# Performance work log

Measured on AMD Instinct MI355X. Metric: run time of the kernel, lower is better.

The kernel has to match this reference:

```python
import jax, jax.numpy as jnp
import numpy as np

V, N, D, R, L, KS = 32000, 2048, 1024, 16, 4, 7
B, H = 2, 4 * 1024
GMIN, GMAX, ACAP = 0.85, 1.0, 1.0


def rmsnorm(x, w, eps=1e-6):
    return x * jax.lax.rsqrt(jnp.mean(x * x, axis=-1, keepdims=True) + eps) * w


def l2norm(x, eps=1e-8):
    return x / jnp.maximum(jnp.linalg.norm(x, axis=-1, keepdims=True), eps)


def mlp(x, w1, b1, w2, b2):
    return jax.nn.gelu(x @ w1 + b1) @ w2 + b2


def k1_block(h, nw, w1, b1, w2, b2):
    return h + mlp(rmsnorm(h, nw), w1, b1, w2, b2)


def causal_conv(h, kernel):
    # depthwise causal conv with shared 1D kernel; kernel[0] = current step
    n = h.shape[1]
    hp = jnp.pad(h, ((0, 0), (KS - 1, 0), (0, 0)))
    out = jnp.zeros_like(h)
    for k in range(KS):  # KS is small & static
        out = out + kernel[k] * hp[:, KS - 1 - k: KS - 1 - k + n, :]
    return out


def k2_layer(h, p):
    (u, v, dlog, alog, glog, kern, pw, pb, n1w, n2w, w1, b1, w2, b2) = p
    residual = h
    hn = rmsnorm(h, n1w)
    gate = jax.nn.sigmoid(glog)
    out = gate * causal_conv(hn, kern)
    # low-rank q/k
    q = l2norm(hn @ u)          # (B,N,R)
    k = l2norm(hn @ v)          # (B,N,R)
    gamma = GMIN + (GMAX - GMIN) * jax.nn.sigmoid(dlog)   # (R,)
    alpha = ACAP * jax.nn.sigmoid(alog)                   # (R,)
    qa = q * alpha
    pos = jnp.arange(h.shape[1])
    diff = jnp.maximum(pos[:, None] - pos[None, :], 0).astype(h.dtype)
    mask = (pos[:, None] >= pos[None, :]).astype(h.dtype)
    # per-rank causal decay matrix gamma_r^(i-j): (R,N,N)
    decay = jnp.exp(diff[None] * jnp.log(gamma)[:, None, None]) * mask[None]
    scores = jnp.einsum('bir,rij,bjr->bij', qa, decay, k)  # (B,N,N)
    out = out + jnp.einsum('bij,bjd->bid', scores, hn)
    out = out @ pw + pb
    h = residual + out
    h = h + mlp(rmsnorm(h, n2w), w1, b1, w2, b2)
    return h


def setup_inputs() -> dict:
    key = jax.random.key(0)
    ks = jax.random.split(key, 32)
    f32 = jnp.float32
    inp = {
        'tokens': jax.random.randint(ks[0], (B, N), 0, V),
        'emb_table': jax.random.normal(ks[1], (V, D), f32) * 0.02,
        'k1a_nw': jnp.ones((D,), f32),
        'k1a_w1': jax.random.normal(ks[2], (D, H), f32) * 0.02,
        'k1a_b1': jnp.zeros((H,), f32),
        'k1a_w2': jax.random.normal(ks[3], (H, D), f32) * 0.02,
        'k1a_b2': jnp.zeros((D,), f32),
        'k2_u': jax.random.normal(ks[4], (L, D, R), f32) * 0.05,
        'k2_v': jax.random.normal(ks[5], (L, D, R), f32) * 0.05,
        'k2_dlog': jax.random.normal(ks[6], (L, R), f32) * 0.5,
        'k2_alog': jnp.zeros((L, R), f32),
        'k2_glog': jnp.zeros((L,), f32),
        'k2_kern': jax.random.normal(ks[7], (L, KS), f32) * 0.1,
        'k2_pw': jax.random.normal(ks[8], (L, D, D), f32) * 0.02,
        'k2_pb': jnp.zeros((L, D), f32),
        'k2_n1w': jnp.ones((L, D), f32),
        'k2_n2w': jnp.ones((L, D), f32),
        'k2_w1': jax.random.normal(ks[9], (L, D, H), f32) * 0.02,
        'k2_b1': jnp.zeros((L, H), f32),
        'k2_w2': jax.random.normal(ks[10], (L, H, D), f32) * 0.02,
        'k2_b2': jnp.zeros((L, D), f32),
        'k1b_nw': jnp.ones((D,), f32),
        'k1b_w1': jax.random.normal(ks[11], (D, H), f32) * 0.02,
        'k1b_b1': jnp.zeros((H,), f32),
        'k1b_w2': jax.random.normal(ks[12], (H, D), f32) * 0.02,
        'k1b_b2': jnp.zeros((D,), f32),
        'k0_nw': jnp.ones((D,), f32),
        'head_w': jax.random.normal(ks[13], (D, V), f32) * 0.02,
        'head_b': jnp.zeros((V,), f32),
    }
    return inp


def reference(tokens, emb_table,
              k1a_nw, k1a_w1, k1a_b1, k1a_w2, k1a_b2,
              k2_u, k2_v, k2_dlog, k2_alog, k2_glog, k2_kern,
              k2_pw, k2_pb, k2_n1w, k2_n2w, k2_w1, k2_b1, k2_w2, k2_b2,
              k1b_nw, k1b_w1, k1b_b1, k1b_w2, k1b_b2,
              k0_nw, head_w, head_b):
    h = emb_table[tokens]                                  # (B,N,D)
    h = k1_block(h, k1a_nw, k1a_w1, k1a_b1, k1a_w2, k1a_b2)
    stacked = (k2_u, k2_v, k2_dlog, k2_alog, k2_glog, k2_kern,
               k2_pw, k2_pb, k2_n1w, k2_n2w, k2_w1, k2_b1, k2_w2, k2_b2)
    def step(c, p):
        return k2_layer(c, p), None
    h, _ = jax.lax.scan(step, h, stacked)
    h = k1_block(h, k1b_nw, k1b_w1, k1b_b1, k1b_w2, k1b_b2)
    h = rmsnorm(h, k0_nw)                                  # K0 final norm
    return h @ head_w + head_b                             # (B,N,V)
```

## Files before the change

kernel.cpp:

```cpp
#include <hip/hip_runtime.h>
#include <hip/hip_bf16.h>

#define SEQ 2048
#define DIM 1024
#define RNK 16
#define NL 4
#define KT 7
#define BATCH 2
#define HID 4096
#define VOC 32000
#define BNROWS (BATCH*SEQ)
#define CHK 128
#define NCH (SEQ/CHK)
#define PRMS 128
#define KAPP 160

typedef __hip_bfloat16 bf16;
typedef __attribute__((ext_vector_type(8))) short bh8;
typedef __attribute__((ext_vector_type(4))) float vf4;

__device__ __forceinline__ float bfu(unsigned int u) { u <<= 16; return __builtin_bit_cast(float, u); }
__device__ __forceinline__ unsigned short f2bu(float x) { bf16 t = __float2bfloat16(x); return __builtin_bit_cast(unsigned short, t); }
__device__ __forceinline__ float b2f(bf16 x) { return __bfloat162float(x); }
__device__ __forceinline__ float sigm(float x) { return 1.f / (1.f + expf(-x)); }
__device__ __forceinline__ float gelu_t(float x) {
    float u = 0.7978845608028654f * (x + 0.044715f * x * x * x);
    return 0.5f * x * (1.f + tanhf(u));
}

__device__ __forceinline__ void gld16(const bf16* g, bf16* l) {
    __builtin_amdgcn_global_load_lds(
        (const __attribute__((address_space(1))) void*)g,
        (__attribute__((address_space(3))) void*)l,
        16, 0, 0);
}

__global__ void embed_kernel(const int* __restrict__ tokens, const float* __restrict__ emb,
                             float* __restrict__ h) {
    int row = blockIdx.x;
    int tok = tokens[row];
    const float4* src = (const float4*)(emb + (size_t)tok * DIM);
    float4* dst = (float4*)(h + (size_t)row * DIM);
    dst[threadIdx.x] = src[threadIdx.x];
}

__global__ void rmsnorm_kernel(const float* __restrict__ in, const float* __restrict__ wt,
                               bf16* __restrict__ out) {
    int row = blockIdx.x;
    int tx = threadIdx.x;
    float4 v = ((const float4*)(in + (size_t)row * DIM))[tx];
    float ss = v.x * v.x + v.y * v.y + v.z * v.z + v.w * v.w;
#pragma unroll
    for (int off = 32; off > 0; off >>= 1) ss += __shfl_down(ss, off);
    __shared__ float red[4];
    int lane = tx & 63, wv = tx >> 6;
    if (lane == 0) red[wv] = ss;
    __syncthreads();
    float tot = red[0] + red[1] + red[2] + red[3];
    float scale = rsqrtf(tot * (1.f / DIM) + 1e-6f);
    float4 w4 = ((const float4*)wt)[tx];
    uint2 o;
    o.x = f2bu(v.x * scale * w4.x) | ((unsigned int)f2bu(v.y * scale * w4.y) << 16);
    o.y = f2bu(v.z * scale * w4.z) | ((unsigned int)f2bu(v.w * scale * w4.w) << 16);
    *(uint2*)(out + (size_t)row * DIM + tx * 4) = o;
}

__global__ void transpose_cast_kernel(const float* __restrict__ in, bf16* __restrict__ out,
                                      int K, int Nc) {
    __shared__ float tile[32][33];
    int n0 = blockIdx.x * 32, k0 = blockIdx.y * 32;
    int tx = threadIdx.x & 31, ty = threadIdx.x >> 5;
#pragma unroll
    for (int i = 0; i < 32; i += 8)
        tile[ty + i][tx] = in[(size_t)(k0 + ty + i) * Nc + n0 + tx];
    __syncthreads();
#pragma unroll
    for (int i = 0; i < 32; i += 8)
        out[(size_t)(n0 + ty + i) * K + k0 + tx] = __float2bfloat16(tile[tx][ty + i]);
}

__global__ void prep_kernel(const float* __restrict__ dlog, const float* __restrict__ alog,
                            const float* __restrict__ glog, const float* __restrict__ kern,
                            float* __restrict__ prm) {
    int l = blockIdx.x, t = threadIdx.x;
    float* p = prm + l * PRMS;
    if (t < RNK) {
        float g = 0.85f + 0.15f * sigm(dlog[l * RNK + t]);
        float lg = logf(g);
        p[t] = g;
        p[16 + t] = lg;
        p[32 + t] = expf(lg * (float)CHK);
        p[48 + t] = sigm(alog[l * RNK + t]);
    }
    if (t < KT) {
        float gate = sigm(glog[l]);
        p[64 + t] = gate * kern[l * KT + t];
    }
}

__global__ void prep_uv_kernel(const float* __restrict__ u, const float* __restrict__ v,
                               bf16* __restrict__ uvT) {
    int l = blockIdx.y;
    int k = blockIdx.x * 256 + threadIdx.x;
    const float* ul = u + (size_t)l * DIM * RNK;
    const float* vl = v + (size_t)l * DIM * RNK;
    bf16* o = uvT + (size_t)l * 32 * DIM;
#pragma unroll
    for (int r = 0; r < RNK; ++r) {
        o[(size_t)r * DIM + k] = __float2bfloat16(ul[(size_t)k * RNK + r]);
        o[(size_t)(RNK + r) * DIM + k] = __float2bfloat16(vl[(size_t)k * RNK + r]);
    }
}

__global__ void conv_kernel(const bf16* __restrict__ hn, const float* __restrict__ prm,
                            bf16* __restrict__ Zc) {
    int t = blockIdx.x * 256 + threadIdx.x;
    int d4 = (t & 255) * 4;
    int row = t >> 8;
    int n = row & (SEQ - 1);
    float a0 = 0, a1 = 0, a2 = 0, a3 = 0;
#pragma unroll
    for (int kk = 0; kk < KT; ++kk) {
        if (n - kk < 0) break;
        float wv = prm[64 + kk];
        uint2 hv = *(const uint2*)(hn + (size_t)(row - kk) * DIM + d4);
        a0 += wv * bfu(hv.x & 0xffffu);
        a1 += wv * bfu(hv.x >> 16);
        a2 += wv * bfu(hv.y & 0xffffu);
        a3 += wv * bfu(hv.y >> 16);
    }
    uint2 o;
    o.x = f2bu(a0) | ((unsigned int)f2bu(a1) << 16);
    o.y = f2bu(a2) | ((unsigned int)f2bu(a3) << 16);
    *(uint2*)(Zc + (size_t)row * DIM + d4) = o;
}

__global__ __launch_bounds__(64)
void qk_mfma_kernel(const bf16* __restrict__ hn, const bf16* __restrict__ uvT,
                    const float* __restrict__ prm, float* __restrict__ qa,
                    float* __restrict__ kn) {
    int row0 = blockIdx.x * 16;
    int lane = threadIdx.x;
    int fr = lane & 15, kf = (lane >> 4) * 8;
    vf4 accq = {}, acck = {};
#pragma unroll 4
    for (int kt = 0; kt < DIM / 32; ++kt) {
        int k0 = kt * 32;
        bh8 b0 = *(const bh8*)(uvT + (size_t)fr * DIM + k0 + kf);
        bh8 b1 = *(const bh8*)(uvT + (size_t)(16 + fr) * DIM + k0 + kf);
        bh8 a0 = *(const bh8*)(hn + (size_t)(row0 + fr) * DIM + k0 + kf);
        accq = __builtin_amdgcn_mfma_f32_16x16x32_bf16(a0, b0, accq, 0, 0, 0);
        acck = __builtin_amdgcn_mfma_f32_16x16x32_bf16(a0, b1, acck, 0, 0, 0);
    }
    int fq = lane >> 4;
    float alpha = prm[48 + fr];
#pragma unroll
    for (int j = 0; j < 4; ++j) {
        float qv = accq[j], kv = acck[j];
        float sq = qv * qv, sk = kv * kv;
#pragma unroll
        for (int mask = 1; mask < 16; mask <<= 1) {
            sq += __shfl_xor(sq, mask);
            sk += __shfl_xor(sk, mask);
        }
        int row = row0 + fq * 4 + j;
        qa[(size_t)row * RNK + fr] = qv / fmaxf(sqrtf(sq), 1e-8f) * alpha;
        kn[(size_t)row * RNK + fr] = kv / fmaxf(sqrtf(sk), 1e-8f);
    }
}

__global__ void trans_hn_kernel(const bf16* __restrict__ hn, bf16* __restrict__ HB) {
    __shared__ bf16 tile[32][40];
    int bc = blockIdx.x;
    int d0 = blockIdx.y * 32, j0 = blockIdx.z * 32;
    int tx = threadIdx.x & 31, ty = threadIdx.x >> 5;
    size_t rowb = (size_t)bc * CHK;
#pragma unroll
    for (int i = 0; i < 32; i += 8)
        tile[ty + i][tx] = hn[(rowb + j0 + ty + i) * DIM + d0 + tx];
    __syncthreads();
    bf16* Hp = HB + (size_t)bc * DIM * KAPP;
#pragma unroll
    for (int i = 0; i < 32; i += 8)
        Hp[(size_t)(d0 + ty + i) * KAPP + j0 + tx] = tile[tx][ty + i];
}

__global__ void scores_kernel(const float* __restrict__ qa, const float* __restrict__ kn,
                              const float* __restrict__ prm, bf16* __restrict__ SA,
                              bf16* __restrict__ kdtB) {
    int bc = blockIdx.x;
    int yt = blockIdx.y;
    __shared__ float ptab[CHK][16];
    for (int e = threadIdx.x; e < CHK * 16; e += 256) {
        int tt = e >> 4, r = e & 15;
        ptab[tt][r] = expf(prm[16 + r] * (float)tt);
    }
    __syncthreads();
    size_t rowb = (size_t)bc * CHK;
    bf16* SAp = SA + (size_t)bc * CHK * KAPP;
    for (int e = threadIdx.x; e < 16 * CHK; e += 256) {
        int i = yt * 16 + (e >> 7), j = e & (CHK - 1);
        float vsum = 0.f;
        if (i >= j) {
            const float* qp = qa + (rowb + i) * RNK;
            const float* kp = kn + (rowb + j) * RNK;
#pragma unroll
            for (int r = 0; r < 16; ++r) vsum += qp[r] * ptab[i - j][r] * kp[r];
        }
        SAp[(size_t)i * KAPP + j] = __float2bfloat16(vsum);
    }
    for (int e = threadIdx.x; e < 16 * 32; e += 256) {
        int i = yt * 16 + (e >> 5), rr = e & 31;
        float w = 0.f;
        if (rr < 16) w = qa[(rowb + i) * RNK + rr] * expf(prm[16 + rr] * (float)(i + 1));
        SAp[(size_t)i * KAPP + CHK + rr] = __float2bfloat16(w);
    }
    bf16* kp2 = kdtB + (size_t)bc * RNK * CHK;
    for (int e = threadIdx.x; e < 2 * CHK; e += 256) {
        int r = 2 * yt + (e >> 7), j = e & (CHK - 1);
        kp2[(size_t)r * CHK + j] =
            __float2bfloat16(ptab[CHK - 1 - j][r] * kn[(rowb + j) * RNK + r]);
    }
}

__global__ __launch_bounds__(64)
void chunkU_kernel(const bf16* __restrict__ HB, const bf16* __restrict__ kdtB,
                   float* __restrict__ U) {
    int bc = blockIdx.x;
    int d0 = blockIdx.y * 64;
    int lane = threadIdx.x;
    int fr = lane & 15, kf = (lane >> 4) * 8;
    const bf16* Hp = HB + (size_t)bc * DIM * KAPP;
    const bf16* Kp = kdtB + (size_t)bc * RNK * CHK;
    vf4 acc[4] = {};
#pragma unroll
    for (int kt = 0; kt < 4; ++kt) {
        int k0 = kt * 32;
        bh8 bb = *(const bh8*)(Kp + (size_t)fr * CHK + k0 + kf);
#pragma unroll
        for (int m = 0; m < 4; ++m) {
            bh8 a = *(const bh8*)(Hp + (size_t)(d0 + m * 16 + fr) * KAPP + k0 + kf);
            acc[m] = __builtin_amdgcn_mfma_f32_16x16x32_bf16(a, bb, acc[m], 0, 0, 0);
        }
    }
    int fq = lane >> 4;
    float* Up = U + (size_t)bc * DIM * RNK;
#pragma unroll
    for (int m = 0; m < 4; ++m)
#pragma unroll
        for (int j = 0; j < 4; ++j)
            Up[(size_t)(d0 + m * 16 + fq * 4 + j) * RNK + fr] = acc[m][j];
}

__global__ void scanP_kernel(const float* __restrict__ U, const float* __restrict__ prm,
                             bf16* __restrict__ HB) {
    int g = blockIdx.x * 256 + threadIdx.x;
    int rq = g & 3;
    int d = (g >> 2) & (DIM - 1);
    int b = g >> 12;
    float gC[4], p[4];
#pragma unroll
    for (int q = 0; q < 4; ++q) { gC[q] = prm[32 + rq * 4 + q]; p[q] = 0.f; }
    for (int c = 0; c < NCH; ++c) {
        int bc = b * NCH + c;
        uint2 pk;
        pk.x = (unsigned int)f2bu(p[0]) | ((unsigned int)f2bu(p[1]) << 16);
        pk.y = (unsigned int)f2bu(p[2]) | ((unsigned int)f2bu(p[3]) << 16);
        *(uint2*)(HB + (size_t)bc * DIM * KAPP + (size_t)d * KAPP + CHK + rq * 4) = pk;
        float4 u4 = *(const float4*)(U + ((size_t)bc * DIM + d) * RNK + rq * 4);
        p[0] = gC[0] * p[0] + u4.x;
        p[1] = gC[1] * p[1] + u4.y;
        p[2] = gC[2] * p[2] + u4.z;
        p[3] = gC[3] * p[3] + u4.w;
    }
}

__global__ __launch_bounds__(256)
void apply_gemm_kernel(const bf16* __restrict__ SA, const bf16* __restrict__ HB,
                       const bf16* __restrict__ Zc, bf16* __restrict__ Zb) {
    __shared__ alignas(16) bf16 As[128][40];
    __shared__ alignas(16) bf16 Bs[128][40];
    int bc = blockIdx.y;
    int colB0 = blockIdx.x * 128;
    int t = threadIdx.x;
    int lane = t & 63, wid = t >> 6;
    int wr = wid >> 1, wc = wid & 1;
    vf4 acc[4][4] = {};
    const bf16* A = SA + (size_t)bc * CHK * KAPP;
    const bf16* BT = HB + (size_t)bc * DIM * KAPP;
    int r1 = t >> 2, ko1 = (t & 3) * 8;
    int fr = lane & 15, kf = (lane >> 4) * 8;
#pragma unroll
    for (int kt = 0; kt < 5; ++kt) {
        int k0 = kt * 32;
        int4 va1 = *(const int4*)(A + (size_t)r1 * KAPP + k0 + ko1);
        int4 va2 = *(const int4*)(A + (size_t)(r1 + 64) * KAPP + k0 + ko1);
        int4 vb1 = *(const int4*)(BT + (size_t)(colB0 + r1) * KAPP + k0 + ko1);
        int4 vb2 = *(const int4*)(BT + (size_t)(colB0 + r1 + 64) * KAPP + k0 + ko1);
        __syncthreads();
        *(int4*)&As[r1][ko1] = va1;
        *(int4*)&As[r1 + 64][ko1] = va2;
        *(int4*)&Bs[r1][ko1] = vb1;
        *(int4*)&Bs[r1 + 64][ko1] = vb2;
        __syncthreads();
        bh8 a[4], bb[4];
#pragma unroll
        for (int m = 0; m < 4; ++m) a[m] = *(const bh8*)&As[wr * 64 + m * 16 + fr][kf];
#pragma unroll
        for (int n = 0; n < 4; ++n) bb[n] = *(const bh8*)&Bs[wc * 64 + n * 16 + fr][kf];
#pragma unroll
        for (int m = 0; m < 4; ++m)
#pragma unroll
            for (int n = 0; n < 4; ++n)
                acc[m][n] = __builtin_amdgcn_mfma_f32_16x16x32_bf16(a[m], bb[n], acc[m][n], 0, 0, 0);
    }
    int fq = lane >> 4;
    size_t rowb = (size_t)bc * CHK;
#pragma unroll
    for (int m = 0; m < 4; ++m) {
#pragma unroll
        for (int n = 0; n < 4; ++n) {
            int col = colB0 + wc * 64 + n * 16 + fr;
#pragma unroll
            for (int j = 0; j < 4; ++j) {
                size_t row = rowb + wr * 64 + m * 16 + fq * 4 + j;
                size_t idx = row * DIM + col;
                Zb[idx] = __float2bfloat16(b2f(Zc[idx]) + acc[m][n][j]);
            }
        }
    }
}

template <int EPI>
__global__ __launch_bounds__(256)
void gemm_kernel(const bf16* __restrict__ A, const bf16* __restrict__ BT,
                 const float* __restrict__ bias, const float* __restrict__ res,
                 float* __restrict__ outF, bf16* __restrict__ outB,
                 int M, int Nc, int K, int lda) {
    __shared__ alignas(16) bf16 As[128][32];
    __shared__ alignas(16) bf16 Bs[128][32];
    int gx = gridDim.x;
    int orig = blockIdx.y * gx + blockIdx.x;
    int qch = (gx * gridDim.y) >> 3;
    int wg = (orig & 7) * qch + (orig >> 3);
    int bn = wg % gx, bm = wg / gx;
    int t = threadIdx.x;
    int lane = t & 63, wid = t >> 6;
    int wr = wid >> 1, wc = wid & 1;
    vf4 acc[4][4] = {};
    const int rowA0 = bm * 128, colB0 = bn * 128;
    int fr = lane & 15, kf = (lane >> 4) * 8;
    int c0 = wid * 2;
    int lrow = lane >> 2;
    int lcol = (lane & 3) * 8;
    const bf16* Ag0 = A + (size_t)(rowA0 + c0 * 16 + lrow) * lda + lcol;
    const bf16* Ag1 = A + (size_t)(rowA0 + c0 * 16 + 16 + lrow) * lda + lcol;
    const bf16* Bg0 = BT + (size_t)(colB0 + c0 * 16 + lrow) * lda + lcol;
    const bf16* Bg1 = BT + (size_t)(colB0 + c0 * 16 + 16 + lrow) * lda + lcol;
    bf16* Al0 = &As[0][0] + c0 * 512;
    bf16* Al1 = Al0 + 512;
    bf16* Bl0 = &Bs[0][0] + c0 * 512;
    bf16* Bl1 = Bl0 + 512;
    int nk = K >> 5;
    for (int kt = 0; kt < nk; ++kt) {
        int k0 = kt * 32;
        __syncthreads();
        gld16(Ag0 + k0, Al0);
        gld16(Ag1 + k0, Al1);
        gld16(Bg0 + k0, Bl0);
        gld16(Bg1 + k0, Bl1);
        asm volatile("s_waitcnt vmcnt(0)" ::: "memory");
        __syncthreads();
        bh8 a[4], bb[4];
#pragma unroll
        for (int m = 0; m < 4; ++m) a[m] = *(const bh8*)&As[wr * 64 + m * 16 + fr][kf];
#pragma unroll
        for (int n = 0; n < 4; ++n) bb[n] = *(const bh8*)&Bs[wc * 64 + n * 16 + fr][kf];
#pragma unroll
        for (int m = 0; m < 4; ++m)
#pragma unroll
            for (int n = 0; n < 4; ++n)
                acc[m][n] = __builtin_amdgcn_mfma_f32_16x16x32_bf16(a[m], bb[n], acc[m][n], 0, 0, 0);
    }
    int fq = lane >> 4;
#pragma unroll
    for (int m = 0; m < 4; ++m) {
#pragma unroll
        for (int n = 0; n < 4; ++n) {
            int col = colB0 + wc * 64 + n * 16 + fr;
            float bv = bias[col];
#pragma unroll
            for (int j = 0; j < 4; ++j) {
                int row = rowA0 + wr * 64 + m * 16 + fq * 4 + j;
                size_t idx = (size_t)row * Nc + col;
                float v2 = acc[m][n][j] + bv;
                if (EPI == 1) v2 += res[idx];
                outF[idx] = v2;
            }
        }
    }
}

#define SB __builtin_amdgcn_sched_barrier(0)
template <int EPI>
__global__ __launch_bounds__(512, 2)
void gemm256_kernel(const bf16* __restrict__ A, const bf16* __restrict__ BT,
                    const float* __restrict__ bias,
                    float* __restrict__ outF, bf16* __restrict__ outB,
                    int M, int Nc, int K, int lda) {
    extern __shared__ char smem[];
    bf16* Alds = (bf16*)smem;
    bf16* Blds = (bf16*)(smem + 65536);
    if (EPI == 4) {
        size_t zo = (size_t)blockIdx.z * K;
        A += zo; BT += zo;
        outB += (size_t)blockIdx.z * ((size_t)M * Nc);
    }
    int gx = gridDim.x, gy = gridDim.y;
    int orig = blockIdx.y * gx + blockIdx.x;
    int qch = (gx * gy) >> 3;
    int wg = (orig & 7) * qch + (orig >> 3);
    int bm = wg % gy, bn = wg / gy;
    int rowA0 = bm * 256, colB0 = bn * 256;
    int tid = threadIdx.x;
    int lane = tid & 63, wid = tid >> 6;
    int wm = wid >> 2, wn = wid & 3;
    int fr = lane & 15;
    int kf8 = ((((lane >> 4) & 3) ^ ((fr >> 1) & 3)) * 8);
    int srow = wid * 16 + (lane >> 2);
    int scol = (((lane & 3) ^ ((lane >> 3) & 3)) * 8);
    const bf16* Ags = A + (size_t)(rowA0 + srow) * lda + scol;
    const bf16* Bgs = BT + (size_t)(colB0 + srow) * lda + scol;
    int sbase = wid * 512;
    auto stA = [&](int d, int kh, int k0) {
        bf16* dst = Alds + (d * 2 + kh) * 8192 + sbase;
        const bf16* src = Ags + k0 + kh * 32;
        gld16(src, dst);
        gld16(src + (size_t)128 * lda, dst + 4096);
    };
    auto stB = [&](int d, int kh, int k0) {
        bf16* dst = Blds + (d * 2 + kh) * 8192 + sbase;
        const bf16* src = Bgs + k0 + kh * 32;
        gld16(src, dst);
        gld16(src + (size_t)128 * lda, dst + 4096);
    };
    const bf16* Ard = Alds + (size_t)(wm * 128 + fr) * 32 + kf8;
    const bf16* Brd = Blds + (size_t)(wn * 64 + fr) * 32 + kf8;
    vf4 acc[8][4] = {};
    int ntk = K >> 6;
    stB(0, 0, 0); stB(0, 1, 0); stA(0, 0, 0); stA(0, 1, 0);
    for (int t = 0; t < ntk; ++t) {
        int d = t & 1, nd = d ^ 1;
        int k1 = (t + 1) << 6;
        bool pf = (t + 1 < ntk);
        int dof = d * 16384;
        int dof1 = dof + 8192;
        bh8 bF0[4], bF1[4];
        if (pf) { stB(nd, 0, k1); stB(nd, 1, k1);
                  asm volatile("s_waitcnt vmcnt(4)" ::: "memory"); }
        else    { asm volatile("s_waitcnt vmcnt(0)" ::: "memory"); }
        SB; __builtin_amdgcn_s_barrier(); SB;
        {
            bh8 a00 = *(const bh8*)(Ard + dof + 0 * 512);
            bh8 a01 = *(const bh8*)(Ard + dof + 1 * 512);
            bh8 a02 = *(const bh8*)(Ard + dof + 2 * 512);
            bh8 a03 = *(const bh8*)(Ard + dof + 3 * 512);
            bh8 a10 = *(const bh8*)(Ard + dof1 + 0 * 512);
            bh8 a11 = *(const bh8*)(Ard + dof1 + 1 * 512);
            bh8 a12 = *(const bh8*)(Ard + dof1 + 2 * 512);
            bh8 a13 = *(const bh8*)(Ard + dof1 + 3 * 512);
#pragma unroll
            for (int n = 0; n < 4; ++n) {
                bF0[n] = *(const bh8*)(Brd + dof + n * 512);
                bF1[n] = *(const bh8*)(Brd + dof1 + n * 512);
            }
            __builtin_amdgcn_s_setprio(1);
#pragma unroll
            for (int n = 0; n < 4; ++n) {
                acc[0][n] = __builtin_amdgcn_mfma_f32_16x16x32_bf16(a00, bF0[n], acc[0][n], 0, 0, 0);
                acc[1][n] = __builtin_amdgcn_mfma_f32_16x16x32_bf16(a01, bF0[n], acc[1][n], 0, 0, 0);
                acc[2][n] = __builtin_amdgcn_mfma_f32_16x16x32_bf16(a02, bF0[n], acc[2][n], 0, 0, 0);
                acc[3][n] = __builtin_amdgcn_mfma_f32_16x16x32_bf16(a03, bF0[n], acc[3][n], 0, 0, 0);
            }
#pragma unroll
            for (int n = 0; n < 4; ++n) {
                acc[0][n] = __builtin_amdgcn_mfma_f32_16x16x32_bf16(a10, bF1[n], acc[0][n], 0, 0, 0);
                acc[1][n] = __builtin_amdgcn_mfma_f32_16x16x32_bf16(a11, bF1[n], acc[1][n], 0, 0, 0);
                acc[2][n] = __builtin_amdgcn_mfma_f32_16x16x32_bf16(a12, bF1[n], acc[2][n], 0, 0, 0);
                acc[3][n] = __builtin_amdgcn_mfma_f32_16x16x32_bf16(a13, bF1[n], acc[3][n], 0, 0, 0);
            }
            __builtin_amdgcn_s_setprio(0);
        }
        SB;
        if (pf) { stA(nd, 0, k1); stA(nd, 1, k1); }
        SB; __builtin_amdgcn_s_barrier(); SB;
        {
            bh8 a00 = *(const bh8*)(Ard + dof + 4 * 512);
            bh8 a01 = *(const bh8*)(Ard + dof + 5 * 512);
            bh8 a02 = *(const bh8*)(Ard + dof + 6 * 512);
            bh8 a03 = *(const bh8*)(Ard + dof + 7 * 512);
            bh8 a10 = *(const bh8*)(Ard + dof1 + 4 * 512);
            bh8 a11 = *(const bh8*)(Ard + dof1 + 5 * 512);
            bh8 a12 = *(const bh8*)(Ard + dof1 + 6 * 512);
            bh8 a13 = *(const bh8*)(Ard + dof1 + 7 * 512);
            __builtin_amdgcn_s_setprio(1);
#pragma unroll
            for (int n = 0; n < 4; ++n) {
                acc[4][n] = __builtin_amdgcn_mfma_f32_16x16x32_bf16(a00, bF0[n], acc[4][n], 0, 0, 0);
                acc[5][n] = __builtin_amdgcn_mfma_f32_16x16x32_bf16(a01, bF0[n], acc[5][n], 0, 0, 0);
                acc[6][n] = __builtin_amdgcn_mfma_f32_16x16x32_bf16(a02, bF0[n], acc[6][n], 0, 0, 0);
                acc[7][n] = __builtin_amdgcn_mfma_f32_16x16x32_bf16(a03, bF0[n], acc[7][n], 0, 0, 0);
            }
#pragma unroll
            for (int n = 0; n < 4; ++n) {
                acc[4][n] = __builtin_amdgcn_mfma_f32_16x16x32_bf16(a10, bF1[n], acc[4][n], 0, 0, 0);
                acc[5][n] = __builtin_amdgcn_mfma_f32_16x16x32_bf16(a11, bF1[n], acc[5][n], 0, 0, 0);
                acc[6][n] = __builtin_amdgcn_mfma_f32_16x16x32_bf16(a12, bF1[n], acc[6][n], 0, 0, 0);
                acc[7][n] = __builtin_amdgcn_mfma_f32_16x16x32_bf16(a13, bF1[n], acc[7][n], 0, 0, 0);
            }
            __builtin_amdgcn_s_setprio(0);
        }
        SB;
    }
    int fq = lane >> 4;
    if (EPI == 0) {
        __syncthreads();
        float* W = (float*)smem + wid * 1024;
        int rr = lane >> 3;
        int cb = (lane & 7) * 4;
#pragma unroll
        for (int mi = 0; mi < 8; ++mi) {
#pragma unroll
            for (int ni = 0; ni < 4; ++ni)
#pragma unroll
                for (int j = 0; j < 4; ++j)
                    W[(fq * 4 + j) * 64 + ni * 16 + fr] = acc[mi][ni][j];
#pragma unroll
            for (int p = 0; p < 2; ++p) {
#pragma unroll
                for (int q = 0; q < 2; ++q) {
                    vf4 v = *(vf4*)&W[(p * 8 + rr) * 64 + q * 32 + cb];
                    int col = colB0 + wn * 64 + q * 32 + cb;
                    int row = rowA0 + wm * 128 + mi * 16 + p * 8 + rr;
                    vf4 bv4 = *(const vf4*)&bias[col];
                    v += bv4;
                    __builtin_nontemporal_store(v, (vf4*)&outF[(size_t)row * Nc + col]);
                }
            }
            __syncthreads();
        }
    } else {
#pragma unroll
        for (int mi = 0; mi < 8; ++mi) {
#pragma unroll
            for (int ni = 0; ni < 4; ++ni) {
                int col = colB0 + wn * 64 + ni * 16 + fr;
                float bv = (EPI == 4) ? 0.f : bias[col];
#pragma unroll
                for (int j = 0; j < 4; ++j) {
                    int row = rowA0 + wm * 128 + mi * 16 + fq * 4 + j;
                    size_t idx = (size_t)row * Nc + col;
                    float v2 = acc[mi][ni][j] + bv;
                    if (EPI == 2) outB[idx] = __float2bfloat16(gelu_t(v2));
                    else outB[idx] = __float2bfloat16(v2);
                }
            }
        }
    }
}

__global__ void combine4_norm_kernel(const bf16* __restrict__ P, const float* __restrict__ bias,
                                     const float* __restrict__ nw, float* __restrict__ h,
                                     bf16* __restrict__ hnb) {
    int row = blockIdx.x;
    int tx = threadIdx.x;
    const size_t S = (size_t)BNROWS * DIM;
    size_t base = (size_t)row * DIM + tx * 4;
    float4 hv = *(float4*)(h + base);
    float4 bv = ((const float4*)bias)[tx];
    float s0 = bv.x, s1 = bv.y, s2 = bv.z, s3 = bv.w;
#pragma unroll
    for (int q = 0; q < 4; ++q) {
        uint2 pk = *(const uint2*)(P + q * S + base);
        s0 += bfu(pk.x & 0xffffu);
        s1 += bfu(pk.x >> 16);
        s2 += bfu(pk.y & 0xffffu);
        s3 += bfu(pk.y >> 16);
    }
    hv.x += s0; hv.y += s1; hv.z += s2; hv.w += s3;
    *(float4*)(h + base) = hv;
    float ss = hv.x * hv.x + hv.y * hv.y + hv.z * hv.z + hv.w * hv.w;
#pragma unroll
    for (int off = 32; off > 0; off >>= 1) ss += __shfl_down(ss, off);
    __shared__ float red[4];
    int lane = tx & 63, wv = tx >> 6;
    if (lane == 0) red[wv] = ss;
    __syncthreads();
    float tot = red[0] + red[1] + red[2] + red[3];
    float scale = rsqrtf(tot * (1.f / DIM) + 1e-6f);
    float4 w4 = ((const float4*)nw)[tx];
    uint2 o;
    o.x = f2bu(hv.x * scale * w4.x) | ((unsigned int)f2bu(hv.y * scale * w4.y) << 16);
    o.y = f2bu(hv.z * scale * w4.z) | ((unsigned int)f2bu(hv.w * scale * w4.w) << 16);
    *(uint2*)(hnb + (size_t)row * DIM + tx * 4) = o;
}

extern "C" void kernel_launch(void* const* d_in, const int* in_sizes, int n_in,
                              void* d_out, int out_size, void* d_ws, size_t ws_size,
                              hipStream_t stream) {
    (void)in_sizes; (void)n_in; (void)out_size; (void)ws_size;
    const int* tokens = (const int*)d_in[0];
    const float* emb = (const float*)d_in[1];
    const float* k1a_nw = (const float*)d_in[2];
    const float* k1a_w1 = (const float*)d_in[3];
    const float* k1a_b1 = (const float*)d_in[4];
    const float* k1a_w2 = (const float*)d_in[5];
    const float* k1a_b2 = (const float*)d_in[6];
    const float* k2_u = (const float*)d_in[7];
    const float* k2_v = (const float*)d_in[8];
    const float* k2_dlog = (const float*)d_in[9];
    const float* k2_alog = (const float*)d_in[10];
    const float* k2_glog = (const float*)d_in[11];
    const float* k2_kern = (const float*)d_in[12];
    const float* k2_pw = (const float*)d_in[13];
    const float* k2_pb = (const float*)d_in[14];
    const float* k2_n1w = (const float*)d_in[15];
    const float* k2_n2w = (const float*)d_in[16];
    const float* k2_w1 = (const float*)d_in[17];
    const float* k2_b1 = (const float*)d_in[18];
    const float* k2_w2 = (const float*)d_in[19];
    const float* k2_b2 = (const float*)d_in[20];
    const float* k1b_nw = (const float*)d_in[21];
    const float* k1b_w1 = (const float*)d_in[22];
    const float* k1b_b1 = (const float*)d_in[23];
    const float* k1b_w2 = (const float*)d_in[24];
    const float* k1b_b2 = (const float*)d_in[25];
    const float* k0_nw = (const float*)d_in[26];
    const float* head_w = (const float*)d_in[27];
    const float* head_b = (const float*)d_in[28];
    float* out = (float*)d_out;

    (void)hipFuncSetAttribute((const void*)gemm256_kernel<0>,
                              hipFuncAttributeMaxDynamicSharedMemorySize, 131072);
    (void)hipFuncSetAttribute((const void*)gemm256_kernel<2>,
                              hipFuncAttributeMaxDynamicSharedMemorySize, 131072);
    (void)hipFuncSetAttribute((const void*)gemm256_kernel<4>,
                              hipFuncAttributeMaxDynamicSharedMemorySize, 131072);

    char* wsp = (char*)d_ws;
    auto alloc = [&](size_t bytes) -> char* {
        char* p = wsp;
        wsp += (bytes + 255) & ~(size_t)255;
        return p;
    };
    float* h   = (float*)alloc((size_t)BNROWS * DIM * 4);
    bf16* Zc   = (bf16*)alloc((size_t)BNROWS * DIM * 2);
    bf16* hnb  = (bf16*)alloc((size_t)BNROWS * DIM * 2);
    bf16* Zb   = (bf16*)alloc((size_t)BNROWS * DIM * 2);
    bf16* t1b  = (bf16*)alloc((size_t)BNROWS * HID * 2);
    float* qaB = (float*)alloc((size_t)BNROWS * RNK * 4);
    float* knB = (float*)alloc((size_t)BNROWS * RNK * 4);
    float* U   = (float*)alloc((size_t)BATCH * NCH * DIM * RNK * 4);
    bf16* HB   = (bf16*)alloc((size_t)BATCH * NCH * DIM * KAPP * 2);
    bf16* SA   = (bf16*)alloc((size_t)BATCH * NCH * CHK * KAPP * 2);
    bf16* kdtB = (bf16*)alloc((size_t)BATCH * NCH * RNK * CHK * 2);
    float* prm = (float*)alloc((size_t)NL * PRMS * 4);
    bf16* uvT  = (bf16*)alloc((size_t)NL * 32 * DIM * 2);
    bf16* w1aT = (bf16*)alloc((size_t)HID * DIM * 2);
    bf16* w2aT = (bf16*)alloc((size_t)DIM * HID * 2);
    bf16* w1bT = (bf16*)alloc((size_t)HID * DIM * 2);
    bf16* w2bT = (bf16*)alloc((size_t)DIM * HID * 2);
    bf16* pwT  = (bf16*)alloc((size_t)NL * DIM * DIM * 2);
    bf16* w1T  = (bf16*)alloc((size_t)NL * DIM * HID * 2);
    bf16* w2T  = (bf16*)alloc((size_t)NL * HID * DIM * 2);
    bf16* headT = (bf16*)alloc((size_t)VOC * DIM * 2);
    bf16* Pk  = (bf16*)alloc((size_t)4 * BNROWS * DIM * 2);

    hipMemsetAsync(HB, 0, (size_t)BATCH * NCH * DIM * KAPP * 2, stream);

    auto T = [&](const float* in, bf16* o, int K, int Nc) {
        transpose_cast_kernel<<<dim3(Nc / 32, K / 32), 256, 0, stream>>>(in, o, K, Nc);
    };
    T(k1a_w1, w1aT, DIM, HID);
    T(k1a_w2, w2aT, HID, DIM);
    T(k1b_w1, w1bT, DIM, HID);
    T(k1b_w2, w2bT, HID, DIM);
    for (int l = 0; l < NL; ++l) {
        T(k2_pw + (size_t)l * DIM * DIM, pwT + (size_t)l * DIM * DIM, DIM, DIM);
        T(k2_w1 + (size_t)l * DIM * HID, w1T + (size_t)l * DIM * HID, DIM, HID);
        T(k2_w2 + (size_t)l * HID * DIM, w2T + (size_t)l * HID * DIM, HID, DIM);
    }
    T(head_w, headT, DIM, VOC);
    prep_kernel<<<NL, 32, 0, stream>>>(k2_dlog, k2_alog, k2_glog, k2_kern, prm);
    prep_uv_kernel<<<dim3(DIM / 256, NL), 256, 0, stream>>>(k2_u, k2_v, uvT);

    auto mlp_core = [&](const bf16* W1, const float* B1, const bf16* W2, const float* B2,
                        const float* nw_next) {
        gemm256_kernel<2><<<dim3(HID / 256, BNROWS / 256), 512, 131072, stream>>>(
            hnb, W1, B1, nullptr, t1b, BNROWS, HID, DIM, DIM);
        gemm256_kernel<4><<<dim3(DIM / 256, BNROWS / 256, 4), 512, 131072, stream>>>(
            t1b, W2, nullptr, nullptr, Pk, BNROWS, DIM, HID / 4, HID);
        combine4_norm_kernel<<<BNROWS, 256, 0, stream>>>(Pk, B2, nw_next, h, hnb);
    };

    embed_kernel<<<BNROWS, 256, 0, stream>>>(tokens, emb, h);
    rmsnorm_kernel<<<BNROWS, 256, 0, stream>>>(h, k1a_nw, hnb);
    mlp_core(w1aT, k1a_b1, w2aT, k1a_b2, k2_n1w);

    for (int l = 0; l < NL; ++l) {
        const float* prm_l = prm + l * PRMS;
        conv_kernel<<<BNROWS, 256, 0, stream>>>(hnb, prm_l, Zc);
        qk_mfma_kernel<<<BNROWS / 16, 64, 0, stream>>>(hnb, uvT + (size_t)l * 32 * DIM,
                                                       prm_l, qaB, knB);
        trans_hn_kernel<<<dim3(BATCH * NCH, DIM / 32, CHK / 32), 256, 0, stream>>>(hnb, HB);
        scores_kernel<<<dim3(BATCH * NCH, 8), 256, 0, stream>>>(qaB, knB, prm_l, SA, kdtB);
        chunkU_kernel<<<dim3(BATCH * NCH, DIM / 64), 64, 0, stream>>>(HB, kdtB, U);
        scanP_kernel<<<BATCH * DIM * 4 / 256, 256, 0, stream>>>(U, prm_l, HB);
        apply_gemm_kernel<<<dim3(DIM / 128, BATCH * NCH), 256, 0, stream>>>(SA, HB, Zc, Zb);
        gemm_kernel<1><<<dim3(DIM / 128, BNROWS / 128), 256, 0, stream>>>(
            Zb, pwT + (size_t)l * DIM * DIM, k2_pb + (size_t)l * DIM, h, h, nullptr,
            BNROWS, DIM, DIM, DIM);
        rmsnorm_kernel<<<BNROWS, 256, 0, stream>>>(h, k2_n2w + (size_t)l * DIM, hnb);
        const float* nw_next = (l < NL - 1) ? (k2_n1w + (size_t)(l + 1) * DIM) : k1b_nw;
        mlp_core(w1T + (size_t)l * DIM * HID, k2_b1 + (size_t)l * HID,
                 w2T + (size_t)l * HID * DIM, k2_b2 + (size_t)l * DIM, nw_next);
    }

    mlp_core(w1bT, k1b_b1, w2bT, k1b_b2, k0_nw);

    gemm256_kernel<0><<<dim3(VOC / 256, BNROWS / 256), 512, 131072, stream>>>(
        hnb, headT, head_b, out, nullptr, BNROWS, VOC, DIM, DIM);
}
```

Measured before the change: 1.448 ms.

## Switch GEMM mainloop to 4-stage K=32 ring buffer and pad epilogue staging

The GEMM main loop moves from a double-buffered K=64 tile with two barrier phases per step to a 4-slot ring of K=32 slices, keeping three loads in flight and issuing the next prefetch once fragments are in registers. The goal is to hide global-load latency better and reduce stalls between MFMA bursts. The fp32 epilogue staging stride is padded from 64 to 68 floats to avoid LDS bank conflicts, and the per-iteration __syncthreads there is removed. The costs are twice as many loop iterations and barriers per K, and the removed epilogue sync relies on each wave owning its staging region.

```diff
diff --git a/kernel.cpp b/kernel.cpp
--- a/kernel.cpp
+++ b/kernel.cpp
@@ -432,100 +432,72 @@
     const bf16* Ags = A + (size_t)(rowA0 + srow) * lda + scol;
     const bf16* Bgs = BT + (size_t)(colB0 + srow) * lda + scol;
     int sbase = wid * 512;
-    auto stA = [&](int d, int kh, int k0) {
-        bf16* dst = Alds + (d * 2 + kh) * 8192 + sbase;
-        const bf16* src = Ags + k0 + kh * 32;
+    auto stA = [&](int b, int k0) {
+        bf16* dst = Alds + b * 8192 + sbase;
+        const bf16* src = Ags + k0;
         gld16(src, dst);
         gld16(src + (size_t)128 * lda, dst + 4096);
     };
-    auto stB = [&](int d, int kh, int k0) {
-        bf16* dst = Blds + (d * 2 + kh) * 8192 + sbase;
-        const bf16* src = Bgs + k0 + kh * 32;
+    auto stB = [&](int b, int k0) {
+        bf16* dst = Blds + b * 8192 + sbase;
+        const bf16* src = Bgs + k0;
         gld16(src, dst);
         gld16(src + (size_t)128 * lda, dst + 4096);
     };
     const bf16* Ard = Alds + (size_t)(wm * 128 + fr) * 32 + kf8;
     const bf16* Brd = Blds + (size_t)(wn * 64 + fr) * 32 + kf8;
     vf4 acc[8][4] = {};
-    int ntk = K >> 6;
-    stB(0, 0, 0); stB(0, 1, 0); stA(0, 0, 0); stA(0, 1, 0);
+    int ntk = K >> 5;
+    stB(0, 0); stA(0, 0);
+    stB(1, 32); stA(1, 32);
+    stB(2, 64); stA(2, 64);
     for (int t = 0; t < ntk; ++t) {
-        int d = t & 1, nd = d ^ 1;
-        int k1 = (t + 1) << 6;
-        bool pf = (t + 1 < ntk);
-        int dof = d * 16384;
-        int dof1 = dof + 8192;
-        bh8 bF0[4], bF1[4];
-        if (pf) { stB(nd, 0, k1); stB(nd, 1, k1);
-                  asm volatile("s_waitcnt vmcnt(4)" ::: "memory"); }
-        else    { asm volatile("s_waitcnt vmcnt(0)" ::: "memory"); }
+        int b = t & 3;
+        int rem = ntk - 1 - t;
+        int bo = b * 8192;
+        if (rem >= 2)      asm volatile("s_waitcnt vmcnt(8)" ::: "memory");
+        else if (rem == 1) asm volatile("s_waitcnt vmcnt(4)" ::: "memory");
+        else               asm volatile("s_waitcnt vmcnt(0)" ::: "memory");
         SB; __builtin_amdgcn_s_barrier(); SB;
-        {
-            bh8 a00 = *(const bh8*)(Ard + dof + 0 * 512);
-            bh8 a01 = *(const bh8*)(Ard + dof + 1 * 512);
-            bh8 a02 = *(const bh8*)(Ard + dof + 2 * 512);
-            bh8 a03 = *(const bh8*)(Ard + dof + 3 * 512);
-            bh8 a10 = *(const bh8*)(Ard + dof1 + 0 * 512);
-            bh8 a11 = *(const bh8*)(Ard + dof1 + 1 * 512);
-            bh8 a12 = *(const bh8*)(Ard + dof1 + 2 * 512);
-            bh8 a13 = *(const bh8*)(Ard + dof1 + 3 * 512);
-#pragma unroll
-            for (int n = 0; n < 4; ++n) {
-                bF0[n] = *(const bh8*)(Brd + dof + n * 512);
-                bF1[n] = *(const bh8*)(Brd + dof1 + n * 512);
-            }
-            __builtin_amdgcn_s_setprio(1);
-#pragma unroll
-            for (int n = 0; n < 4; ++n) {
-                acc[0][n] = __builtin_amdgcn_mfma_f32_16x16x32_bf16(a00, bF0[n], acc[0][n], 0, 0, 0);
-                acc[1][n] = __builtin_amdgcn_mfma_f32_16x16x32_bf16(a01, bF0[n], acc[1][n], 0, 0, 0);
-                acc[2][n] = __builtin_amdgcn_mfma_f32_16x16x32_bf16(a02, bF0[n], acc[2][n], 0, 0, 0);
-                acc[3][n] = __builtin_amdgcn_mfma_f32_16x16x32_bf16(a03, bF0[n], acc[3][n], 0, 0, 0);
-            }
-#pragma unroll
-            for (int n = 0; n < 4; ++n) {
-                acc[0][n] = __builtin_amdgcn_mfma_f32_16x16x32_bf16(a10, bF1[n], acc[0][n], 0, 0, 0);
-                acc[1][n] = __builtin_amdgcn_mfma_f32_16x16x32_bf16(a11, bF1[n], acc[1][n], 0, 0, 0);
-                acc[2][n] = __builtin_amdgcn_mfma_f32_16x16x32_bf16(a12, bF1[n], acc[2][n], 0, 0, 0);
-                acc[3][n] = __builtin_amdgcn_mfma_f32_16x16x32_bf16(a13, bF1[n], acc[3][n], 0, 0, 0);
-            }
-            __builtin_amdgcn_s_setprio(0);
+        bh8 bF[4], aF[4];
+#pragma unroll
+        for (int n = 0; n < 4; ++n) bF[n] = *(const bh8*)(Brd + bo + n * 512);
+#pragma unroll
+        for (int m = 0; m < 4; ++m) aF[m] = *(const bh8*)(Ard + bo + m * 512);
+        asm volatile("s_waitcnt lgkmcnt(0)" ::: "memory"); SB;
+        __builtin_amdgcn_s_barrier(); SB;
+        if (rem >= 3) {
+            int k3 = (t + 3) << 5;
+            int pb = (t + 3) & 3;
+            stB(pb, k3); stA(pb, k3);
         }
         SB;
-        if (pf) { stA(nd, 0, k1); stA(nd, 1, k1); }
-        SB; __builtin_amdgcn_s_barrier(); SB;
-        {
-            bh8 a00 = *(const bh8*)(Ard + dof + 4 * 512);
-            bh8 a01 = *(const bh8*)(Ard + dof + 5 * 512);
-            bh8 a02 = *(const bh8*)(Ard + dof + 6 * 512);
-            bh8 a03 = *(const bh8*)(Ard + dof + 7 * 512);
-            bh8 a10 = *(const bh8*)(Ard + dof1 + 4 * 512);
-            bh8 a11 = *(const bh8*)(Ard + dof1 + 5 * 512);
-            bh8 a12 = *(const bh8*)(Ard + dof1 + 6 * 512);
-            bh8 a13 = *(const bh8*)(Ard + dof1 + 7 * 512);
-            __builtin_amdgcn_s_setprio(1);
-#pragma unroll
-            for (int n = 0; n < 4; ++n) {
-                acc[4][n] = __builtin_amdgcn_mfma_f32_16x16x32_bf16(a00, bF0[n], acc[4][n], 0, 0, 0);
-                acc[5][n] = __builtin_amdgcn_mfma_f32_16x16x32_bf16(a01, bF0[n], acc[5][n], 0, 0, 0);
-                acc[6][n] = __builtin_amdgcn_mfma_f32_16x16x32_bf16(a02, bF0[n], acc[6][n], 0, 0, 0);
-                acc[7][n] = __builtin_amdgcn_mfma_f32_16x16x32_bf16(a03, bF0[n], acc[7][n], 0, 0, 0);
-            }
-#pragma unroll
-            for (int n = 0; n < 4; ++n) {
-                acc[4][n] = __builtin_amdgcn_mfma_f32_16x16x32_bf16(a10, bF1[n], acc[4][n], 0, 0, 0);
-                acc[5][n] = __builtin_amdgcn_mfma_f32_16x16x32_bf16(a11, bF1[n], acc[5][n], 0, 0, 0);
-                acc[6][n] = __builtin_amdgcn_mfma_f32_16x16x32_bf16(a12, bF1[n], acc[6][n], 0, 0, 0);
-                acc[7][n] = __builtin_amdgcn_mfma_f32_16x16x32_bf16(a13, bF1[n], acc[7][n], 0, 0, 0);
-            }
-            __builtin_amdgcn_s_setprio(0);
-        }
+        __builtin_amdgcn_s_setprio(1);
+#pragma unroll
+        for (int n = 0; n < 4; ++n) {
+            acc[0][n] = __builtin_amdgcn_mfma_f32_16x16x32_bf16(aF[0], bF[n], acc[0][n], 0, 0, 0);
+            acc[1][n] = __builtin_amdgcn_mfma_f32_16x16x32_bf16(aF[1], bF[n], acc[1][n], 0, 0, 0);
+            acc[2][n] = __builtin_amdgcn_mfma_f32_16x16x32_bf16(aF[2], bF[n], acc[2][n], 0, 0, 0);
+            acc[3][n] = __builtin_amdgcn_mfma_f32_16x16x32_bf16(aF[3], bF[n], acc[3][n], 0, 0, 0);
+        }
+        bh8 aG0 = *(const bh8*)(Ard + bo + 4 * 512);
+        bh8 aG1 = *(const bh8*)(Ard + bo + 5 * 512);
+        bh8 aG2 = *(const bh8*)(Ard + bo + 6 * 512);
+        bh8 aG3 = *(const bh8*)(Ard + bo + 7 * 512);
+#pragma unroll
+        for (int n = 0; n < 4; ++n) {
+            acc[4][n] = __builtin_amdgcn_mfma_f32_16x16x32_bf16(aG0, bF[n], acc[4][n], 0, 0, 0);
+            acc[5][n] = __builtin_amdgcn_mfma_f32_16x16x32_bf16(aG1, bF[n], acc[5][n], 0, 0, 0);
+            acc[6][n] = __builtin_amdgcn_mfma_f32_16x16x32_bf16(aG2, bF[n], acc[6][n], 0, 0, 0);
+            acc[7][n] = __builtin_amdgcn_mfma_f32_16x16x32_bf16(aG3, bF[n], acc[7][n], 0, 0, 0);
+        }
+        __builtin_amdgcn_s_setprio(0);
         SB;
     }
     int fq = lane >> 4;
     if (EPI == 0) {
         __syncthreads();
-        float* W = (float*)smem + wid * 1024;
+        float* W = (float*)smem + wid * 1104;
         int rr = lane >> 3;
         int cb = (lane & 7) * 4;
 #pragma unroll
@@ -534,12 +506,12 @@
             for (int ni = 0; ni < 4; ++ni)
 #pragma unroll
                 for (int j = 0; j < 4; ++j)
-                    W[(fq * 4 + j) * 64 + ni * 16 + fr] = acc[mi][ni][j];
+                    W[(fq * 4 + j) * 68 + ni * 16 + fr] = acc[mi][ni][j];
 #pragma unroll
             for (int p = 0; p < 2; ++p) {
 #pragma unroll
                 for (int q = 0; q < 2; ++q) {
-                    vf4 v = *(vf4*)&W[(p * 8 + rr) * 64 + q * 32 + cb];
+                    vf4 v = *(vf4*)&W[(p * 8 + rr) * 68 + q * 32 + cb];
                     int col = colB0 + wn * 64 + q * 32 + cb;
                     int row = rowA0 + wm * 128 + mi * 16 + p * 8 + rr;
                     vf4 bv4 = *(const vf4*)&bias[col];
@@ -547,7 +519,6 @@
                     __builtin_nontemporal_store(v, (vf4*)&outF[(size_t)row * Nc + col]);
                 }
             }
-            __syncthreads();
         }
     } else {
 #pragma unroll
```

Measured after the change: 1.517 ms (median of 2 runs). 4.8% more time.
